# Optimization experiments

Hardware: AMD Instinct MI355X
Metric: run time of the kernel (lower is better)

The kernel has to match this reference:

```python
import jax, jax.numpy as jnp
import numpy as np

N_NODES = 200000
N_EVENTS = 100000
MEM_DIM = 100
TIME_DIM = 100
MSG_DIM = 172
T_MAX = 1000000


def setup_inputs() -> dict:
    key = jax.random.key(0)
    ks = jax.random.split(key, 12)
    s = 0.05
    return {
        "memory": jax.random.normal(ks[0], (N_NODES, MEM_DIM), jnp.float32),
        "raw_msg": jax.random.normal(ks[1], (N_EVENTS, MSG_DIM), jnp.float32),
        "time_w": jax.random.normal(ks[2], (TIME_DIM, 1), jnp.float32) * s,
        "time_b": jax.random.normal(ks[3], (TIME_DIM,), jnp.float32) * s,
        "w_ih": jax.random.normal(ks[4], (3 * MEM_DIM, 2 * MEM_DIM + MSG_DIM + TIME_DIM), jnp.float32) * s,
        "w_hh": jax.random.normal(ks[5], (3 * MEM_DIM, MEM_DIM), jnp.float32) * s,
        "b_ih": jax.random.normal(ks[6], (3 * MEM_DIM,), jnp.float32) * s,
        "b_hh": jax.random.normal(ks[7], (3 * MEM_DIM,), jnp.float32) * s,
        "last_update": jax.random.randint(ks[8], (N_NODES,), 0, T_MAX, jnp.int32),
        "src": jax.random.randint(ks[9], (N_EVENTS,), 0, N_NODES, jnp.int32),
        "dst": jax.random.randint(ks[10], (N_EVENTS,), 0, N_NODES, jnp.int32),
        "t": jax.random.randint(ks[11], (N_EVENTS,), 0, T_MAX, jnp.int32),
    }


def _time_enc(t_rel, time_w, time_b):
    # Linear(1, time_dim) followed by cos, as in TGN.update_memory
    return jnp.cos(t_rel[:, None] * time_w[:, 0][None, :] + time_b[None, :])


def _gru_cell(x, h, w_ih, w_hh, b_ih, b_hh):
    gi = x @ w_ih.T + b_ih  # [N, 3*D]
    gh = h @ w_hh.T + b_hh
    i_r, i_z, i_n = jnp.split(gi, 3, axis=-1)
    h_r, h_z, h_n = jnp.split(gh, 3, axis=-1)
    r = jax.nn.sigmoid(i_r + h_r)
    z = jax.nn.sigmoid(i_z + h_z)
    n = jnp.tanh(i_n + r * h_n)
    return (1.0 - z) * n + z * h


def reference(memory, raw_msg, time_w, time_b, w_ih, w_hh, b_ih, b_hh,
              last_update, src, dst, t):
    # time-relative encodings for source- and destination-side messages
    t_rel_s = (t - last_update[src]).astype(memory.dtype)
    t_rel_d = (t - last_update[dst]).astype(memory.dtype)
    t_enc_s = _time_enc(t_rel_s, time_w, time_b)  # [E, time_dim]
    t_enc_d = _time_enc(t_rel_d, time_w, time_b)

    mem_s = memory[src]  # [E, D]
    mem_d = memory[dst]

    # IdentityMessage: concat(mem_self, mem_other, raw_msg, t_enc)
    msg_s = jnp.concatenate([mem_s, mem_d, raw_msg, t_enc_s], axis=-1)  # [E, 472]
    msg_d = jnp.concatenate([mem_d, mem_s, raw_msg, t_enc_d], axis=-1)

    idx = jnp.concatenate([src, dst], axis=0)          # [2E]
    msgs = jnp.concatenate([msg_s, msg_d], axis=0)      # [2E, 472]

    n_nodes = memory.shape[0]
    # MeanAggregator: per-node mean of incoming messages
    summed = jax.ops.segment_sum(msgs, idx, num_segments=n_nodes)  # [N, 472]
    counts = jax.ops.segment_sum(jnp.ones((idx.shape[0],), memory.dtype), idx,
                                 num_segments=n_nodes)             # [N]
    aggr = summed / jnp.maximum(counts, 1.0)[:, None]

    # GRU memory update, applied only to nodes that received messages
    h_new = _gru_cell(aggr, memory, w_ih, w_hh, b_ih, b_hh)
    touched = (counts > 0)[:, None]
    return jnp.where(touched, h_new, memory)  # [N, memory_dim]
```

## Files before the change

kernel.cpp:

```cpp
#include <hip/hip_runtime.h>
#include <math.h>

#define NND 200000
#define NEV 100000
#define MD 100
#define TD 100
#define MSGD 172
#define NB 64
#define NFRAG 25
#define KS 15
#define BP_ELEMS (KS * NFRAG * 64 * 8)
#define GLS 74

typedef __attribute__((ext_vector_type(8))) short bf16x8;
typedef __attribute__((ext_vector_type(4))) float f32x4;

__device__ __forceinline__ float fast_sigmoid(float x) {
    return 1.0f / (1.0f + __expf(-x));
}
__device__ __forceinline__ float fast_tanh(float x) {
    return fmaf(2.0f, 1.0f / (1.0f + __expf(-2.0f * x)), -1.0f);
}

__device__ __forceinline__ unsigned short f2bf(float f) {
    union { float f; unsigned int u; } v; v.f = f;
    unsigned int r = (v.u + 0x7FFFu + ((v.u >> 16) & 1u)) >> 16;
    return (unsigned short)r;
}
__device__ __forceinline__ float bf2f(unsigned int h) {
    union { unsigned int u; float f; } v; v.u = h << 16;
    return v.f;
}
__device__ __forceinline__ unsigned int pk(float a, float b) {
    unsigned int r;
    asm("v_cvt_pk_bf16_f32 %0, %1, %2" : "=v"(r) : "v"(a), "v"(b));
    return r;
}

__global__ __launch_bounds__(256) void k_scan1(
    const int* __restrict__ cnt, int* __restrict__ off, int* __restrict__ tpos,
    int* __restrict__ psum, int* __restrict__ psumC)
{
    __shared__ int s[5][256];
    int t = threadIdx.x, b = blockIdx.x;
    int i0 = b * 1024 + t * 4;
    int v[4], cls[4];
#pragma unroll
    for (int j = 0; j < 4; ++j) {
        v[j] = (i0 + j < NND) ? cnt[i0 + j] : 0;
        cls[j] = (v[j] == 0) ? -1 : ((v[j] < 4 ? v[j] : 4) - 1);
    }
    int tsum = v[0] + v[1] + v[2] + v[3];
    int fs[4] = {0, 0, 0, 0};
#pragma unroll
    for (int j = 0; j < 4; ++j)
        if (cls[j] >= 0) fs[cls[j]]++;
    s[0][t] = tsum;
#pragma unroll
    for (int X = 0; X < 4; ++X) s[1 + X][t] = fs[X];
    __syncthreads();
    for (int o = 1; o < 256; o <<= 1) {
        int x[5];
#pragma unroll
        for (int ch = 0; ch < 5; ++ch) x[ch] = (t >= o) ? s[ch][t - o] : 0;
        __syncthreads();
#pragma unroll
        for (int ch = 0; ch < 5; ++ch) s[ch][t] += x[ch];
        __syncthreads();
    }
    int e0 = s[0][t] - tsum;
    int eC[4];
#pragma unroll
    for (int X = 0; X < 4; ++X) eC[X] = s[1 + X][t] - fs[X];
    int run = 0;
    int cseen[4] = {0, 0, 0, 0};
#pragma unroll
    for (int j = 0; j < 4; ++j) {
        int i = i0 + j;
        if (i < NND) {
            off[i] = e0 + run;
            if (cls[j] >= 0) tpos[i] = eC[cls[j]] + cseen[cls[j]];
        }
        run += v[j];
        if (cls[j] >= 0) cseen[cls[j]]++;
    }
    if (t == 255) {
        psum[b] = s[0][255];
#pragma unroll
        for (int X = 0; X < 4; ++X) psumC[X * 256 + b] = s[1 + X][255];
    }
}

__global__ __launch_bounds__(256) void k_scan2(
    int* __restrict__ psum, int* __restrict__ psumC,
    int* __restrict__ clsBase, int* __restrict__ ntp, int nblk)
{
    __shared__ int s[5][256];
    int t = threadIdx.x;
    int v[5];
    v[0] = (t < nblk) ? psum[t] : 0;
#pragma unroll
    for (int X = 0; X < 4; ++X) v[1 + X] = (t < nblk) ? psumC[X * 256 + t] : 0;
#pragma unroll
    for (int ch = 0; ch < 5; ++ch) s[ch][t] = v[ch];
    __syncthreads();
    for (int o = 1; o < 256; o <<= 1) {
        int x[5];
#pragma unroll
        for (int ch = 0; ch < 5; ++ch) x[ch] = (t >= o) ? s[ch][t - o] : 0;
        __syncthreads();
#pragma unroll
        for (int ch = 0; ch < 5; ++ch) s[ch][t] += x[ch];
        __syncthreads();
    }
    if (t < nblk) {
        psum[t] = s[0][t] - v[0];
#pragma unroll
        for (int X = 0; X < 4; ++X) psumC[X * 256 + t] = s[1 + X][t] - v[1 + X];
    }
    if (t == 0) {
        int T0 = s[1][nblk - 1], T1 = s[2][nblk - 1];
        int T2 = s[3][nblk - 1], T3 = s[4][nblk - 1];
        clsBase[0] = 0;
        clsBase[1] = T0;
        clsBase[2] = T0 + T1;
        clsBase[3] = T0 + T1 + T2;
        ntp[0] = T0 + T1 + T2 + T3;
    }
}

__global__ __launch_bounds__(256) void k_scan3(
    const int* __restrict__ cnt, int* __restrict__ off, int* __restrict__ tpos,
    const int* __restrict__ psum, const int* __restrict__ psumC,
    const int* __restrict__ clsBase, int* __restrict__ cur)
{
    int t = threadIdx.x, b = blockIdx.x;
    int base = psum[b];
    int i0 = b * 1024 + t * 4;
#pragma unroll
    for (int j = 0; j < 4; ++j) {
        int i = i0 + j;
        if (i < NND) {
            int v = off[i] + base;
            off[i] = v;
            cur[i] = v;
            int c = cnt[i];
            if (c > 0) {
                int cls = (c < 4 ? c : 4) - 1;
                tpos[i] = clsBase[cls] + psumC[cls * 256 + b] + tpos[i];
            }
        }
    }
}

__global__ __launch_bounds__(256) void k_convert(
    const float* __restrict__ w_ih, const float* __restrict__ w_hh,
    const float* __restrict__ raw_msg,
    const int* __restrict__ src, const int* __restrict__ dst,
    unsigned short* __restrict__ Bp, uint4* __restrict__ rawbf,
    int* __restrict__ cnt)
{
    int idx = blockIdx.x * 256 + threadIdx.x;
    if (idx < BP_ELEMS) {
        int e = idx & 7;
        int lane = (idx >> 3) & 63;
        int t = idx >> 9;
        int nf = t % 25;
        int ks = t / 25;
        int col = nf * 16 + (lane & 15);
        int k = ks * 32 + ((lane >> 4) << 3) + e;
        float v = 0.0f;
        if (col < 200) {
            if (k < 472) v = w_ih[col * 472 + k];
            if (k < 100) v += w_hh[col * 100 + k];
        } else if (col < 300) {
            if (k < 472) v = w_ih[col * 472 + k];
        } else {
            if (k < 100) v = w_hh[(col - 100) * 100 + k];
        }
        Bp[idx] = f2bf(v);
        return;
    }
    int j = idx - BP_ELEMS;
    if (j < NEV * 22) {
        int e = j / 22, r = j - e * 22;
        const float4* rs = reinterpret_cast<const float4*>(raw_msg + (size_t)e * MSGD);
        float4 x = rs[2 * r];
        float4 y = (float4){0.f, 0.f, 0.f, 0.f};
        if (2 * r + 1 < 43) y = rs[2 * r + 1];
        uint4 o;
        o.x = pk(x.x, x.y); o.y = pk(x.z, x.w);
        o.z = pk(y.x, y.y); o.w = pk(y.z, y.w);
        rawbf[j] = o;
        return;
    }
    j -= NEV * 22;
    if (j < NEV) {
        atomicAdd(&cnt[src[j]], 1);
        atomicAdd(&cnt[dst[j]], 1);
    }
}

__global__ __launch_bounds__(256) void k_placecopy(
    const float* __restrict__ memory, const int* __restrict__ cnt,
    const int* __restrict__ off, const int* __restrict__ tpos,
    const int* __restrict__ src, const int* __restrict__ dst,
    const int* __restrict__ tarr, const int* __restrict__ last_update,
    int* __restrict__ cur, float* __restrict__ out,
    uint4* __restrict__ membf, int4* __restrict__ tinfo, int4* __restrict__ entries)
{
    int idx = blockIdx.x * 256 + threadIdx.x;
    if (idx < NND * 13) {
        int node = idx / 13, u = idx - node * 13;
        int c = cnt[node];
        const float4* ms = reinterpret_cast<const float4*>(memory + (size_t)node * MD);
        uint4 o = (uint4){0u, 0u, 0u, 0u};
        if (u < 12) {
            float4 x = ms[2 * u], y = ms[2 * u + 1];
            o.x = pk(x.x, x.y); o.y = pk(x.z, x.w);
            o.z = pk(y.x, y.y); o.w = pk(y.z, y.w);
            if (c == 0) {
                float4* o4 = reinterpret_cast<float4*>(out) + (size_t)node * 25;
                o4[2 * u] = x;
                o4[2 * u + 1] = y;
            }
        } else {
            float4 x = ms[24];
            o.x = pk(x.x, x.y); o.y = pk(x.z, x.w);
            if (c == 0) {
                reinterpret_cast<float4*>(out)[(size_t)node * 25 + 24] = x;
            }
        }
        membf[idx] = o;
        if (c > 0 && u == 0) {
            tinfo[tpos[node]] = make_int4(node, c, off[node], 0);
        }
        return;
    }
    int e = idx - NND * 13;
    if (e < NEV) {
        int s = src[e], d = dst[e], tt = tarr[e];
        int slot = atomicAdd(&cur[s], 1);
        entries[slot] = make_int4(d, e, __float_as_int((float)(tt - last_update[s])), s);
        slot = atomicAdd(&cur[d], 1);
        entries[slot] = make_int4(s, e, __float_as_int((float)(tt - last_update[d])), d);
    }
}

__global__ __launch_bounds__(256) void k_tenc(
    const int4* __restrict__ entries, const float* __restrict__ time_w,
    const float* __restrict__ time_b, unsigned int* __restrict__ tencbf)
{
    int slot = blockIdx.x * 2 + (threadIdx.x >> 7);
    int k = threadIdx.x & 127;
    if (k >= 50) return;
    float trel = __int_as_float(entries[slot].z);
    float2 w = *reinterpret_cast<const float2*>(time_w + 2 * k);
    float2 b = *reinterpret_cast<const float2*>(time_b + 2 * k);
    tencbf[(size_t)slot * 50 + k] =
        pk(__cosf(fmaf(trel, w.x, b.x)), __cosf(fmaf(trel, w.y, b.y)));
}

__global__ __launch_bounds__(512, 4) void tgn_gemm(
    const uint4* __restrict__ membf, const uint4* __restrict__ rawbf,
    const unsigned int* __restrict__ tencbf, const int4* __restrict__ entries,
    const unsigned short* __restrict__ Bp,
    const float* __restrict__ b_ih, const float* __restrict__ b_hh,
    const int* __restrict__ ntp, const int4* __restrict__ tinfo,
    float* __restrict__ out)
{
    __shared__ __align__(16) unsigned short lds[64 * 480];
    __shared__ int node_s[NB], cnt_s[NB], off_s[NB];
    int tid = threadIdx.x;
    int n0 = blockIdx.x * NB;
    int nt = ntp[0];
    if (n0 >= nt) return;

    if (tid < NB) {
        int slot = n0 + tid;
        if (slot < nt) {
            int4 ti = tinfo[slot];
            node_s[tid] = ti.x; cnt_s[tid] = ti.y; off_s[tid] = ti.z;
        } else {
            node_s[tid] = -1; cnt_s[tid] = 0; off_s[tid] = 0;
        }
    }
    __syncthreads();

    int lane = tid & 63;
    int wv = tid >> 6;

    {
        int u = lane;
        const char* membc = reinterpret_cast<const char*>(membf);
        const char* rawbc = reinterpret_cast<const char*>(rawbf);
        const char* tencbc = reinterpret_cast<const char*>(tencbf);
        int selA = 3, selB = 3, strA = 0, strB = 0;
        const char* bA = membc;
        const char* bB = membc;
        if (u == 12) { selB = 0; strB = 208; bB = membc; }
        else if (u >= 13 && u <= 24) { selA = selB = 0; strA = strB = 208; bA = membc + 16 * u - 200; bB = bA + 8; }
        else if (u >= 25 && u <= 45) { selA = selB = 1; strA = strB = 352; bA = rawbc + 16 * u - 400; bB = bA + 8; }
        else if (u == 46) { selA = 1; strA = 352; bA = rawbc + 336; selB = 2; strB = 200; bB = tencbc; }
        else if (u >= 47 && u <= 58) { selA = selB = 2; strA = strB = 200; bA = tencbc + 16 * u - 744; bB = bA + 8; }
        bool enA = (selA != 3), enB = (selB != 3);

        auto gidx = [](int sel, int4 e, int slotId) {
            return (sel == 0) ? e.x : ((sel == 1) ? e.y : slotId);
        };

#pragma unroll
        for (int half = 0; half < 2; ++half) {
            int rb = wv * 8 + half * 4;
            int cc[4], oo[4];
#pragma unroll
            for (int r = 0; r < 4; ++r) { cc[r] = cnt_s[rb + r]; oo[r] = off_s[rb + r]; }
            int maxc = max(max(cc[0], cc[1]), max(cc[2], cc[3]));
            int4 en[4];
#pragma unroll
            for (int r = 0; r < 4; ++r)
                en[r] = (cc[r] > 0) ? entries[oo[r]] : make_int4(0, 0, 0, 0);
            uint4 mreg[4];
#pragma unroll
            for (int r = 0; r < 4; ++r) {
                int nd = node_s[rb + r];
                mreg[r] = (u < 13 && nd >= 0) ? membf[(size_t)nd * 13 + u]
                                              : (uint4){0u, 0u, 0u, 0u};
            }
            uint2 gA[4], gB[4];
#pragma unroll
            for (int r = 0; r < 4; ++r) {
                gA[r] = (uint2){0u, 0u}; gB[r] = (uint2){0u, 0u};
                if (cc[r] > 0) {
                    if (enA) gA[r] = *reinterpret_cast<const uint2*>(
                        bA + (size_t)gidx(selA, en[r], oo[r]) * strA);
                    if (enB) gB[r] = *reinterpret_cast<const uint2*>(
                        bB + (size_t)gidx(selB, en[r], oo[r]) * strB);
                }
            }
            if (maxc <= 1) {
#pragma unroll
                for (int r = 0; r < 4; ++r) {
                    uint4 o;
                    if (u < 12)       o = mreg[r];
                    else if (u == 12) o = (uint4){mreg[r].x, mreg[r].y, gB[r].x, gB[r].y};
                    else              o = (uint4){gA[r].x, gA[r].y, gB[r].x, gB[r].y};
                    if (u < 60) {
                        int nl = rb + r;
                        int byte = (nl * 960 + 16 * u) ^ ((nl & 7) << 4);
                        *reinterpret_cast<uint4*>(reinterpret_cast<char*>(lds) + byte) = o;
                    }
                }
            } else {
                float ac[4][8];
#pragma unroll
                for (int r = 0; r < 4; ++r) {
                    ac[r][0] = bf2f(gA[r].x & 0xffffu); ac[r][1] = bf2f(gA[r].x >> 16);
                    ac[r][2] = bf2f(gA[r].y & 0xffffu); ac[r][3] = bf2f(gA[r].y >> 16);
                    ac[r][4] = bf2f(gB[r].x & 0xffffu); ac[r][5] = bf2f(gB[r].x >> 16);
                    ac[r][6] = bf2f(gB[r].y & 0xffffu); ac[r][7] = bf2f(gB[r].y >> 16);
                }
                for (int j = 1; j < maxc; ++j) {
                    int sl[4];
                    int4 e2[4];
#pragma unroll
                    for (int r = 0; r < 4; ++r) {
                        sl[r] = oo[r] + ((j < cc[r]) ? j : 0);
                        e2[r] = entries[sl[r]];
                    }
                    uint2 hA[4], hB[4];
#pragma unroll
                    for (int r = 0; r < 4; ++r) {
                        hA[r] = (uint2){0u, 0u}; hB[r] = (uint2){0u, 0u};
                        if (j < cc[r]) {
                            if (enA) hA[r] = *reinterpret_cast<const uint2*>(
                                bA + (size_t)gidx(selA, e2[r], sl[r]) * strA);
                            if (enB) hB[r] = *reinterpret_cast<const uint2*>(
                                bB + (size_t)gidx(selB, e2[r], sl[r]) * strB);
                        }
                    }
#pragma unroll
                    for (int r = 0; r < 4; ++r) {
                        if (j < cc[r]) {
                            ac[r][0] += bf2f(hA[r].x & 0xffffu); ac[r][1] += bf2f(hA[r].x >> 16);
                            ac[r][2] += bf2f(hA[r].y & 0xffffu); ac[r][3] += bf2f(hA[r].y >> 16);
                            ac[r][4] += bf2f(hB[r].x & 0xffffu); ac[r][5] += bf2f(hB[r].x >> 16);
                            ac[r][6] += bf2f(hB[r].y & 0xffffu); ac[r][7] += bf2f(hB[r].y >> 16);
                        }
                    }
                }
#pragma unroll
                for (int r = 0; r < 4; ++r) {
                    float ci = 1.0f / fmaxf((float)cc[r], 1.0f);
                    uint4 o;
                    if (u < 12) {
                        o = mreg[r];
                    } else {
                        o.x = (u == 12) ? mreg[r].x : pk(ac[r][0] * ci, ac[r][1] * ci);
                        o.y = (u == 12) ? mreg[r].y : pk(ac[r][2] * ci, ac[r][3] * ci);
                        o.z = pk(ac[r][4] * ci, ac[r][5] * ci);
                        o.w = pk(ac[r][6] * ci, ac[r][7] * ci);
                    }
                    if (u < 60) {
                        int nl = rb + r;
                        int byte = (nl * 960 + 16 * u) ^ ((nl & 7) << 4);
                        *reinterpret_cast<uint4*>(reinterpret_cast<char*>(lds) + byte) = o;
                    }
                }
            }
        }
    }
    __syncthreads();

    int l15 = lane & 15;
    int kg8 = (lane >> 4) << 3;
    int f0 = (wv == 0) ? 0 : (4 + 3 * (wv - 1));
    int cw = (wv == 0) ? 4 : 3;

    f32x4 acc[4][4];
#pragma unroll
    for (int g = 0; g < 4; ++g)
#pragma unroll
        for (int i = 0; i < 4; ++i) acc[g][i] = (f32x4){0.f, 0.f, 0.f, 0.f};

    const bf16x8* BpB = reinterpret_cast<const bf16x8*>(Bp);
    const char* ldsc = reinterpret_cast<const char*>(lds);

#pragma unroll
    for (int ks = 0; ks < KS; ++ks) {
        int k0 = ks * 32 + kg8;
        const bf16x8* bp = BpB + ((size_t)(ks * NFRAG + f0)) * 64 + lane;
        bf16x8 b[4];
#pragma unroll
        for (int i = 0; i < 4; ++i)
            if (i < cw) b[i] = bp[i * 64];
#pragma unroll
        for (int g = 0; g < 4; ++g) {
            int r = g * 16 + l15;
            int ab = (r * 960 + 2 * k0) ^ ((r & 7) << 4);
            bf16x8 a = *reinterpret_cast<const bf16x8*>(ldsc + ab);
#pragma unroll
            for (int i = 0; i < 4; ++i)
                if (i < cw)
                    acc[g][i] = __builtin_amdgcn_mfma_f32_16x16x32_bf16(a, b[i], acc[g][i], 0, 0, 0);
        }
    }

    float mv[13];
    {
        const char* membc = reinterpret_cast<const char*>(membf);
#pragma unroll
        for (int t = 0; t < 13; ++t) {
            int idx = tid + t * 512;
            mv[t] = 0.f;
            if (idx < NB * MD) {
                int n = idx / MD, j = idx - n * MD;
                int nd = node_s[n];
                if (nd >= 0) {
                    unsigned short h = *reinterpret_cast<const unsigned short*>(
                        membc + (size_t)nd * 208 + 2 * j);
                    mv[t] = bf2f((unsigned int)h);
                }
            }
        }
    }

    __syncthreads();

    unsigned short* Gl = lds;
    int kq = (lane >> 4) << 2;
#pragma unroll
    for (int i = 0; i < 4; ++i) {
        if (i < cw) {
            int col = (f0 + i) * 16 + l15;
            float bias = (col < 200) ? (b_ih[col] + b_hh[col])
                       : (col < 300) ? b_ih[col] : b_hh[col - 100];
#pragma unroll
            for (int g = 0; g < 4; ++g) {
                int node = g * 16 + kq;
#pragma unroll
                for (int rp = 0; rp < 2; ++rp) {
                    *reinterpret_cast<unsigned int*>(&Gl[col * GLS + node + 2 * rp]) =
                        pk(acc[g][i][2 * rp] + bias, acc[g][i][2 * rp + 1] + bias);
                }
            }
        }
    }
    __syncthreads();

#pragma unroll
    for (int t = 0; t < 13; ++t) {
        int idx = tid + t * 512;
        if (idx < NB * MD) {
            int n = idx / MD, j = idx - n * MD;
            int nd = node_s[n];
            if (nd >= 0) {
                float rp = bf2f((unsigned int)Gl[j * GLS + n]);
                float zp = bf2f((unsigned int)Gl[(100 + j) * GLS + n]);
                float inp = bf2f((unsigned int)Gl[(200 + j) * GLS + n]);
                float hnp = bf2f((unsigned int)Gl[(300 + j) * GLS + n]);
                float r = fast_sigmoid(rp);
                float z = fast_sigmoid(zp);
                float nn = fast_tanh(fmaf(r, hnp, inp));
                float h = (1.0f - z) * nn + z * mv[t];
                out[(size_t)nd * MD + j] = h;
            }
        }
    }
}

extern "C" void kernel_launch(void* const* d_in, const int* in_sizes, int n_in,
                              void* d_out, int out_size, void* d_ws, size_t ws_size,
                              hipStream_t stream)
{
    const float* memory      = (const float*)d_in[0];
    const float* raw_msg     = (const float*)d_in[1];
    const float* time_w      = (const float*)d_in[2];
    const float* time_b      = (const float*)d_in[3];
    const float* w_ih        = (const float*)d_in[4];
    const float* w_hh        = (const float*)d_in[5];
    const float* b_ih        = (const float*)d_in[6];
    const float* b_hh        = (const float*)d_in[7];
    const int*   last_update = (const int*)d_in[8];
    const int*   src         = (const int*)d_in[9];
    const int*   dst         = (const int*)d_in[10];
    const int*   tarr        = (const int*)d_in[11];
    float* out = (float*)d_out;

    int* cnt     = (int*)d_ws;
    int* off     = cnt + NND;
    int* cur     = off + NND;
    int* tpos    = cur + NND;
    int* psum    = tpos + NND;
    int* psumC   = psum + 256;
    int* clsBase = psumC + 1024;
    int* ntp     = clsBase + 4;
    int4* entries = (int4*)(ntp + 4);
    int4* tinfo = entries + 2 * NEV;
    unsigned int* tencbf = (unsigned int*)(tinfo + NND);
    uint4* membf = (uint4*)(tencbf + (size_t)2 * NEV * 50);
    uint4* rawbf = membf + (size_t)NND * 13;
    unsigned short* Bp = (unsigned short*)(rawbf + (size_t)NEV * 22);
    size_t need = (size_t)((char*)(Bp + BP_ELEMS) - (char*)d_ws);
    if (ws_size < need) return;

    const int NBLK = (NND + 1023) / 1024;
    const int NTILE = NND / NB;
    const int CVT_TOTAL = BP_ELEMS + NEV * 22 + NEV;
    const int PC_TOTAL = NND * 13 + NEV;

    hipMemsetAsync(cnt, 0, NND * sizeof(int), stream);
    k_convert<<<(CVT_TOTAL + 255) / 256, 256, 0, stream>>>(w_ih, w_hh, raw_msg,
                                                           src, dst, Bp, rawbf, cnt);
    k_scan1<<<NBLK, 256, 0, stream>>>(cnt, off, tpos, psum, psumC);
    k_scan2<<<1, 256, 0, stream>>>(psum, psumC, clsBase, ntp, NBLK);
    k_scan3<<<NBLK, 256, 0, stream>>>(cnt, off, tpos, psum, psumC, clsBase, cur);
    k_placecopy<<<(PC_TOTAL + 255) / 256, 256, 0, stream>>>(memory, cnt, off, tpos,
                                                            src, dst, tarr, last_update,
                                                            cur, out, membf, tinfo, entries);
    k_tenc<<<NEV, 256, 0, stream>>>(entries, time_w, time_b, tencbf);
    tgn_gemm<<<NTILE, 512, 0, stream>>>(membf, rawbf, tencbf, entries,
                                        Bp, b_ih, b_hh, ntp, tinfo, out);
}
```

Measured before the change: 243.4 us.

## Read raw_msg fp32 directly in gather and fuse time encoding into placement

Removes the separate raw_msg-to-bf16 conversion pass. The GEMM gather now reads fp32 raw messages directly and packs them to bf16 when staging into LDS. It also drops the k_tenc kernel by computing the cosine time encodings inside k_placecopy, where one thread writes both 50-word rows for each event. This saves one kernel launch and a full write-then-read of the raw buffer. In exchange, the gather reads twice as many bytes for raw lanes, and the tenc work now runs as a serial per-thread loop with scattered stores.

```diff
diff --git a/kernel.cpp b/kernel.cpp
--- a/kernel.cpp
+++ b/kernel.cpp
@@ -155,10 +155,8 @@
 
 __global__ __launch_bounds__(256) void k_convert(
     const float* __restrict__ w_ih, const float* __restrict__ w_hh,
-    const float* __restrict__ raw_msg,
     const int* __restrict__ src, const int* __restrict__ dst,
-    unsigned short* __restrict__ Bp, uint4* __restrict__ rawbf,
-    int* __restrict__ cnt)
+    unsigned short* __restrict__ Bp, int* __restrict__ cnt)
 {
     int idx = blockIdx.x * 256 + threadIdx.x;
     if (idx < BP_ELEMS) {
@@ -182,19 +180,6 @@
         return;
     }
     int j = idx - BP_ELEMS;
-    if (j < NEV * 22) {
-        int e = j / 22, r = j - e * 22;
-        const float4* rs = reinterpret_cast<const float4*>(raw_msg + (size_t)e * MSGD);
-        float4 x = rs[2 * r];
-        float4 y = (float4){0.f, 0.f, 0.f, 0.f};
-        if (2 * r + 1 < 43) y = rs[2 * r + 1];
-        uint4 o;
-        o.x = pk(x.x, x.y); o.y = pk(x.z, x.w);
-        o.z = pk(y.x, y.y); o.w = pk(y.z, y.w);
-        rawbf[j] = o;
-        return;
-    }
-    j -= NEV * 22;
     if (j < NEV) {
         atomicAdd(&cnt[src[j]], 1);
         atomicAdd(&cnt[dst[j]], 1);
@@ -206,8 +191,10 @@
     const int* __restrict__ off, const int* __restrict__ tpos,
     const int* __restrict__ src, const int* __restrict__ dst,
     const int* __restrict__ tarr, const int* __restrict__ last_update,
+    const float* __restrict__ time_w, const float* __restrict__ time_b,
     int* __restrict__ cur, float* __restrict__ out,
-    uint4* __restrict__ membf, int4* __restrict__ tinfo, int4* __restrict__ entries)
+    uint4* __restrict__ membf, int4* __restrict__ tinfo, int4* __restrict__ entries,
+    unsigned int* __restrict__ tencbf)
 {
     int idx = blockIdx.x * 256 + threadIdx.x;
     if (idx < NND * 13) {
@@ -240,29 +227,25 @@
     int e = idx - NND * 13;
     if (e < NEV) {
         int s = src[e], d = dst[e], tt = tarr[e];
-        int slot = atomicAdd(&cur[s], 1);
-        entries[slot] = make_int4(d, e, __float_as_int((float)(tt - last_update[s])), s);
-        slot = atomicAdd(&cur[d], 1);
-        entries[slot] = make_int4(s, e, __float_as_int((float)(tt - last_update[d])), d);
-    }
-}
-
-__global__ __launch_bounds__(256) void k_tenc(
-    const int4* __restrict__ entries, const float* __restrict__ time_w,
-    const float* __restrict__ time_b, unsigned int* __restrict__ tencbf)
-{
-    int slot = blockIdx.x * 2 + (threadIdx.x >> 7);
-    int k = threadIdx.x & 127;
-    if (k >= 50) return;
-    float trel = __int_as_float(entries[slot].z);
-    float2 w = *reinterpret_cast<const float2*>(time_w + 2 * k);
-    float2 b = *reinterpret_cast<const float2*>(time_b + 2 * k);
-    tencbf[(size_t)slot * 50 + k] =
-        pk(__cosf(fmaf(trel, w.x, b.x)), __cosf(fmaf(trel, w.y, b.y)));
+        float trs = (float)(tt - last_update[s]);
+        float trd = (float)(tt - last_update[d]);
+        int slot1 = atomicAdd(&cur[s], 1);
+        entries[slot1] = make_int4(d, e, __float_as_int(trs), s);
+        int slot2 = atomicAdd(&cur[d], 1);
+        entries[slot2] = make_int4(s, e, __float_as_int(trd), d);
+        unsigned int* t1 = tencbf + (size_t)slot1 * 50;
+        unsigned int* t2 = tencbf + (size_t)slot2 * 50;
+        for (int k = 0; k < 50; ++k) {
+            float2 w = *reinterpret_cast<const float2*>(time_w + 2 * k);
+            float2 b = *reinterpret_cast<const float2*>(time_b + 2 * k);
+            t1[k] = pk(__cosf(fmaf(trs, w.x, b.x)), __cosf(fmaf(trs, w.y, b.y)));
+            t2[k] = pk(__cosf(fmaf(trd, w.x, b.x)), __cosf(fmaf(trd, w.y, b.y)));
+        }
+    }
 }
 
 __global__ __launch_bounds__(512, 4) void tgn_gemm(
-    const uint4* __restrict__ membf, const uint4* __restrict__ rawbf,
+    const uint4* __restrict__ membf, const float* __restrict__ raw_msg,
     const unsigned int* __restrict__ tencbf, const int4* __restrict__ entries,
     const unsigned short* __restrict__ Bp,
     const float* __restrict__ b_ih, const float* __restrict__ b_hh,
@@ -293,21 +276,16 @@
     {
         int u = lane;
         const char* membc = reinterpret_cast<const char*>(membf);
-        const char* rawbc = reinterpret_cast<const char*>(rawbf);
         const char* tencbc = reinterpret_cast<const char*>(tencbf);
-        int selA = 3, selB = 3, strA = 0, strB = 0;
-        const char* bA = membc;
-        const char* bB = membc;
-        if (u == 12) { selB = 0; strB = 208; bB = membc; }
-        else if (u >= 13 && u <= 24) { selA = selB = 0; strA = strB = 208; bA = membc + 16 * u - 200; bB = bA + 8; }
-        else if (u >= 25 && u <= 45) { selA = selB = 1; strA = strB = 352; bA = rawbc + 16 * u - 400; bB = bA + 8; }
-        else if (u == 46) { selA = 1; strA = 352; bA = rawbc + 336; selB = 2; strB = 200; bB = tencbc; }
-        else if (u >= 47 && u <= 58) { selA = selB = 2; strA = strB = 200; bA = tencbc + 16 * u - 744; bB = bA + 8; }
-        bool enA = (selA != 3), enB = (selB != 3);
-
-        auto gidx = [](int sel, int4 e, int slotId) {
-            return (sel == 0) ? e.x : ((sel == 1) ? e.y : slotId);
-        };
+        const char* rawc = reinterpret_cast<const char*>(raw_msg);
+        bool isMix  = (u == 12);
+        bool isOth  = (u >= 13 && u <= 24);
+        bool isRawW = (u >= 25 && u <= 45);
+        bool isRawT = (u == 46);
+        bool isTen  = (u >= 47 && u <= 58);
+        int offOth = 16 * u - 200;
+        int offRaw = 32 * u - 800;
+        int offTen = 16 * u - 744;
 
 #pragma unroll
         for (int half = 0; half < 2; ++half) {
@@ -327,24 +305,44 @@
                 mreg[r] = (u < 13 && nd >= 0) ? membf[(size_t)nd * 13 + u]
                                               : (uint4){0u, 0u, 0u, 0u};
             }
-            uint2 gA[4], gB[4];
+            uint2 nA[4], nB[4];
+            float4 wA[4], wB[4];
 #pragma unroll
             for (int r = 0; r < 4; ++r) {
-                gA[r] = (uint2){0u, 0u}; gB[r] = (uint2){0u, 0u};
+                nA[r] = (uint2){0u, 0u}; nB[r] = (uint2){0u, 0u};
+                wA[r] = (float4){0.f, 0.f, 0.f, 0.f}; wB[r] = wA[r];
                 if (cc[r] > 0) {
-                    if (enA) gA[r] = *reinterpret_cast<const uint2*>(
-                        bA + (size_t)gidx(selA, en[r], oo[r]) * strA);
-                    if (enB) gB[r] = *reinterpret_cast<const uint2*>(
-                        bB + (size_t)gidx(selB, en[r], oo[r]) * strB);
+                    if (isOth) {
+                        const char* p = membc + (size_t)en[r].x * 208 + offOth;
+                        nA[r] = *reinterpret_cast<const uint2*>(p);
+                        nB[r] = *reinterpret_cast<const uint2*>(p + 8);
+                    } else if (isMix) {
+                        nB[r] = *reinterpret_cast<const uint2*>(membc + (size_t)en[r].x * 208);
+                    } else if (isRawW) {
+                        const char* p = rawc + (size_t)en[r].y * 688 + offRaw;
+                        wA[r] = *reinterpret_cast<const float4*>(p);
+                        wB[r] = *reinterpret_cast<const float4*>(p + 16);
+                    } else if (isRawT) {
+                        wA[r] = *reinterpret_cast<const float4*>(rawc + (size_t)en[r].y * 688 + 672);
+                        nB[r] = *reinterpret_cast<const uint2*>(tencbc + (size_t)oo[r] * 200);
+                    } else if (isTen) {
+                        const char* p = tencbc + (size_t)oo[r] * 200 + offTen;
+                        nA[r] = *reinterpret_cast<const uint2*>(p);
+                        nB[r] = *reinterpret_cast<const uint2*>(p + 8);
+                    }
                 }
             }
             if (maxc <= 1) {
 #pragma unroll
                 for (int r = 0; r < 4; ++r) {
                     uint4 o;
-                    if (u < 12)       o = mreg[r];
-                    else if (u == 12) o = (uint4){mreg[r].x, mreg[r].y, gB[r].x, gB[r].y};
-                    else              o = (uint4){gA[r].x, gA[r].y, gB[r].x, gB[r].y};
+                    if (u < 12)        o = mreg[r];
+                    else if (isMix)    o = (uint4){mreg[r].x, mreg[r].y, nB[r].x, nB[r].y};
+                    else if (isRawW)   o = (uint4){pk(wA[r].x, wA[r].y), pk(wA[r].z, wA[r].w),
+                                                   pk(wB[r].x, wB[r].y), pk(wB[r].z, wB[r].w)};
+                    else if (isRawT)   o = (uint4){pk(wA[r].x, wA[r].y), pk(wA[r].z, wA[r].w),
+                                                   nB[r].x, nB[r].y};
+                    else               o = (uint4){nA[r].x, nA[r].y, nB[r].x, nB[r].y};
                     if (u < 60) {
                         int nl = rb + r;
                         int byte = (nl * 960 + 16 * u) ^ ((nl & 7) << 4);
@@ -353,12 +351,23 @@
                 }
             } else {
                 float ac[4][8];
+                bool wide = isRawW || isRawT;
 #pragma unroll
                 for (int r = 0; r < 4; ++r) {
-                    ac[r][0] = bf2f(gA[r].x & 0xffffu); ac[r][1] = bf2f(gA[r].x >> 16);
-                    ac[r][2] = bf2f(gA[r].y & 0xffffu); ac[r][3] = bf2f(gA[r].y >> 16);
-                    ac[r][4] = bf2f(gB[r].x & 0xffffu); ac[r][5] = bf2f(gB[r].x >> 16);
-                    ac[r][6] = bf2f(gB[r].y & 0xffffu); ac[r][7] = bf2f(gB[r].y >> 16);
+                    if (wide) {
+                        ac[r][0] = wA[r].x; ac[r][1] = wA[r].y;
+                        ac[r][2] = wA[r].z; ac[r][3] = wA[r].w;
+                    } else {
+                        ac[r][0] = bf2f(nA[r].x & 0xffffu); ac[r][1] = bf2f(nA[r].x >> 16);
+                        ac[r][2] = bf2f(nA[r].y & 0xffffu); ac[r][3] = bf2f(nA[r].y >> 16);
+                    }
+                    if (isRawW) {
+                        ac[r][4] = wB[r].x; ac[r][5] = wB[r].y;
+                        ac[r][6] = wB[r].z; ac[r][7] = wB[r].w;
+                    } else {
+                        ac[r][4] = bf2f(nB[r].x & 0xffffu); ac[r][5] = bf2f(nB[r].x >> 16);
+                        ac[r][6] = bf2f(nB[r].y & 0xffffu); ac[r][7] = bf2f(nB[r].y >> 16);
+                    }
                 }
                 for (int j = 1; j < maxc; ++j) {
                     int sl[4];
@@ -368,24 +377,48 @@
                         sl[r] = oo[r] + ((j < cc[r]) ? j : 0);
                         e2[r] = entries[sl[r]];
                     }
-                    uint2 hA[4], hB[4];
-#pragma unroll
-                    for (int r = 0; r < 4; ++r) {
-                        hA[r] = (uint2){0u, 0u}; hB[r] = (uint2){0u, 0u};
-                        if (j < cc[r]) {
-                            if (enA) hA[r] = *reinterpret_cast<const uint2*>(
-                                bA + (size_t)gidx(selA, e2[r], sl[r]) * strA);
-                            if (enB) hB[r] = *reinterpret_cast<const uint2*>(
-                                bB + (size_t)gidx(selB, e2[r], sl[r]) * strB);
-                        }
-                    }
 #pragma unroll
                     for (int r = 0; r < 4; ++r) {
                         if (j < cc[r]) {
-                            ac[r][0] += bf2f(hA[r].x & 0xffffu); ac[r][1] += bf2f(hA[r].x >> 16);
-                            ac[r][2] += bf2f(hA[r].y & 0xffffu); ac[r][3] += bf2f(hA[r].y >> 16);
-                            ac[r][4] += bf2f(hB[r].x & 0xffffu); ac[r][5] += bf2f(hB[r].x >> 16);
-                            ac[r][6] += bf2f(hB[r].y & 0xffffu); ac[r][7] += bf2f(hB[r].y >> 16);
+                            if (isOth) {
+                                const char* p = membc + (size_t)e2[r].x * 208 + offOth;
+                                uint2 hA = *reinterpret_cast<const uint2*>(p);
+                                uint2 hB = *reinterpret_cast<const uint2*>(p + 8);
+                                ac[r][0] += bf2f(hA.x & 0xffffu); ac[r][1] += bf2f(hA.x >> 16);
+                                ac[r][2] += bf2f(hA.y & 0xffffu); ac[r][3] += bf2f(hA.y >> 16);
+                                ac[r][4] += bf2f(hB.x & 0xffffu); ac[r][5] += bf2f(hB.x >> 16);
+                                ac[r][6] += bf2f(hB.y & 0xffffu); ac[r][7] += bf2f(hB.y >> 16);
+                            } else if (isMix) {
+                                uint2 hB = *reinterpret_cast<const uint2*>(
+                                    membc + (size_t)e2[r].x * 208);
+                                ac[r][4] += bf2f(hB.x & 0xffffu); ac[r][5] += bf2f(hB.x >> 16);
+                                ac[r][6] += bf2f(hB.y & 0xffffu); ac[r][7] += bf2f(hB.y >> 16);
+                            } else if (isRawW) {
+                                const char* p = rawc + (size_t)e2[r].y * 688 + offRaw;
+                                float4 hA = *reinterpret_cast<const float4*>(p);
+                                float4 hB = *reinterpret_cast<const float4*>(p + 16);
+                                ac[r][0] += hA.x; ac[r][1] += hA.y;
+                                ac[r][2] += hA.z; ac[r][3] += hA.w;
+                                ac[r][4] += hB.x; ac[r][5] += hB.y;
+                                ac[r][6] += hB.z; ac[r][7] += hB.w;
+                            } else if (isRawT) {
+                                float4 hA = *reinterpret_cast<const float4*>(
+                                    rawc + (size_t)e2[r].y * 688 + 672);
+                                uint2 hB = *reinterpret_cast<const uint2*>(
+                                    tencbc + (size_t)sl[r] * 200);
+                                ac[r][0] += hA.x; ac[r][1] += hA.y;
+                                ac[r][2] += hA.z; ac[r][3] += hA.w;
+                                ac[r][4] += bf2f(hB.x & 0xffffu); ac[r][5] += bf2f(hB.x >> 16);
+                                ac[r][6] += bf2f(hB.y & 0xffffu); ac[r][7] += bf2f(hB.y >> 16);
+                            } else if (isTen) {
+                                const char* p = tencbc + (size_t)sl[r] * 200 + offTen;
+                                uint2 hA = *reinterpret_cast<const uint2*>(p);
+                                uint2 hB = *reinterpret_cast<const uint2*>(p + 8);
+                                ac[r][0] += bf2f(hA.x & 0xffffu); ac[r][1] += bf2f(hA.x >> 16);
+                                ac[r][2] += bf2f(hA.y & 0xffffu); ac[r][3] += bf2f(hA.y >> 16);
+                                ac[r][4] += bf2f(hB.x & 0xffffu); ac[r][5] += bf2f(hB.x >> 16);
+                                ac[r][6] += bf2f(hB.y & 0xffffu); ac[r][7] += bf2f(hB.y >> 16);
+                            }
                         }
                     }
                 }
@@ -539,26 +572,25 @@
     int4* tinfo = entries + 2 * NEV;
     unsigned int* tencbf = (unsigned int*)(tinfo + NND);
     uint4* membf = (uint4*)(tencbf + (size_t)2 * NEV * 50);
-    uint4* rawbf = membf + (size_t)NND * 13;
-    unsigned short* Bp = (unsigned short*)(rawbf + (size_t)NEV * 22);
+    unsigned short* Bp = (unsigned short*)(membf + (size_t)NND * 13);
     size_t need = (size_t)((char*)(Bp + BP_ELEMS) - (char*)d_ws);
     if (ws_size < need) return;
 
     const int NBLK = (NND + 1023) / 1024;
     const int NTILE = NND / NB;
-    const int CVT_TOTAL = BP_ELEMS + NEV * 22 + NEV;
+    const int CVT_TOTAL = BP_ELEMS + NEV;
     const int PC_TOTAL = NND * 13 + NEV;
 
     hipMemsetAsync(cnt, 0, NND * sizeof(int), stream);
-    k_convert<<<(CVT_TOTAL + 255) / 256, 256, 0, stream>>>(w_ih, w_hh, raw_msg,
-                                                           src, dst, Bp, rawbf, cnt);
+    k_convert<<<(CVT_TOTAL + 255) / 256, 256, 0, stream>>>(w_ih, w_hh, src, dst, Bp, cnt);
     k_scan1<<<NBLK, 256, 0, stream>>>(cnt, off, tpos, psum, psumC);
     k_scan2<<<1, 256, 0, stream>>>(psum, psumC, clsBase, ntp, NBLK);
     k_scan3<<<NBLK, 256, 0, stream>>>(cnt, off, tpos, psum, psumC, clsBase, cur);
     k_placecopy<<<(PC_TOTAL + 255) / 256, 256, 0, stream>>>(memory, cnt, off, tpos,
                                                             src, dst, tarr, last_update,
-                                                            cur, out, membf, tinfo, entries);
-    k_tenc<<<NEV, 256, 0, stream>>>(entries, time_w, time_b, tencbf);
-    tgn_gemm<<<NTILE, 512, 0, stream>>>(membf, rawbf, tencbf, entries,
+                                                            time_w, time_b,
+                                                            cur, out, membf, tinfo, entries,
+                                                            tencbf);
+    tgn_gemm<<<NTILE, 512, 0, stream>>>(membf, raw_msg, tencbf, entries,
                                         Bp, b_ih, b_hh, ntp, tinfo, out);
 }
```

Measured after the change: 343.5 us. +41.1%, slower.
